# Kernel tuning notes

Hardware: AMD Instinct MI355X
Metric: run time of the kernel (lower is better)

Reference implementation:

```python
import jax, jax.numpy as jnp
import numpy as np
from jax import lax

START, STOP, NTAGS = 18, 19, 20
NEG = -10000.0
V, E, H, L = 100000, 300, 512, 512  # vocab, embed_dim, per-direction hidden, seq_len


def setup_inputs() -> dict:
    key = jax.random.key(0)
    ks = jax.random.split(key, 16)
    f = lambda k, s: jax.random.normal(k, s, dtype=jnp.float32) * 0.05
    trans = jax.random.normal(ks[14], (NTAGS, NTAGS), dtype=jnp.float32)
    trans = trans.at[START, :].set(NEG).at[:, STOP].set(NEG)
    return {
        "sentence": jax.random.randint(ks[0], (L,), 0, V),
        "embed_table": f(ks[1], (V, E)),
        "w_ih_f": f(ks[2], (4 * H, E)), "w_hh_f": f(ks[3], (4 * H, H)),
        "b_ih_f": f(ks[4], (4 * H,)), "b_hh_f": f(ks[5], (4 * H,)),
        "w_ih_b": f(ks[6], (4 * H, E)), "w_hh_b": f(ks[7], (4 * H, H)),
        "b_ih_b": f(ks[8], (4 * H,)), "b_hh_b": f(ks[9], (4 * H,)),
        "h0": f(ks[10], (2, H)), "c0": f(ks[11], (2, H)),
        "w_out": f(ks[12], (NTAGS, 2 * H)), "b_out": f(ks[13], (NTAGS,)),
        "transitions": trans,
    }


def _lstm_dir(x, wih, whh, bih, bhh, h0, c0, reverse):
    # x: [L, E]; PyTorch gate order i, f, g, o
    b = bih + bhh
    def step(carry, xt):
        h, c = carry
        g = xt @ wih.T + h @ whh.T + b  # [4H]
        i, fg, gg, o = jnp.split(g, 4)
        c = jax.nn.sigmoid(fg) * c + jax.nn.sigmoid(i) * jnp.tanh(gg)
        h = jax.nn.sigmoid(o) * jnp.tanh(c)
        return (h, c), h
    _, hs = lax.scan(step, (h0, c0), x, reverse=reverse)
    return hs  # [L, H] in time order


def _lstm_feats(sentence, embed_table, w_ih_f, w_hh_f, b_ih_f, b_hh_f,
                w_ih_b, w_hh_b, b_ih_b, b_hh_b, h0, c0, w_out, b_out):
    x = embed_table[sentence]  # [L, E]
    hf = _lstm_dir(x, w_ih_f, w_hh_f, b_ih_f, b_hh_f, h0[0], c0[0], False)
    hb = _lstm_dir(x, w_ih_b, w_hh_b, b_ih_b, b_hh_b, h0[1], c0[1], True)
    h = jnp.concatenate([hf, hb], axis=-1)  # [L, 2H]
    return h @ w_out.T + b_out  # [L, NTAGS]


def reference(sentence, embed_table, w_ih_f, w_hh_f, b_ih_f, b_hh_f,
              w_ih_b, w_hh_b, b_ih_b, b_hh_b, h0, c0, w_out, b_out, transitions):
    feats = _lstm_feats(sentence, embed_table, w_ih_f, w_hh_f, b_ih_f, b_hh_f,
                        w_ih_b, w_hh_b, b_ih_b, b_hh_b, h0, c0, w_out, b_out)
    init = jnp.full((NTAGS,), NEG, dtype=feats.dtype).at[START].set(0.0)

    def vstep(fv, feat):
        scores = fv[None, :] + transitions  # [next_tag, prev_tag]
        bptr = jnp.argmax(scores, axis=1)
        return jnp.max(scores, axis=1) + feat, bptr

    fv, bptrs = lax.scan(vstep, init, feats)  # bptrs: [L, NTAGS]
    terminal = fv + transitions[STOP]
    best = jnp.argmax(terminal)

    def back(tag, bp):
        # tag is the best tag at step t; bp maps tag_t -> tag_{t-1}
        return bp[tag], tag

    _, path = lax.scan(back, best, bptrs, reverse=True)  # [L] in time order
    return path
```

## Files before the change

kernel.cpp:

```cpp
#include <hip/hip_runtime.h>
#include <math.h>

typedef unsigned long long u64;
typedef unsigned int u32;

#define L 512
#define E 300
#define H 512
#define G4H 2048
#define NTAGS 20
#define START_TAG 18
#define STOP_TAG 19

#define KC 100

#define OFF_XW    0u
#define OFF_HIST  8388608u
#define OFF_HBUF  10485760u
#define OFF_FEATS 10502144u

__global__ __launch_bounds__(256) void k1_xw(
    const int* __restrict__ sentence, const float* __restrict__ embed,
    const float* __restrict__ wih_f, const float* __restrict__ wih_b,
    const float* __restrict__ bih_f, const float* __restrict__ bhh_f,
    const float* __restrict__ bih_b, const float* __restrict__ bhh_b,
    float* __restrict__ xw) {
    __shared__ float wST[KC][68];
    __shared__ float xST[KC][68];
    __shared__ int   sT[64];

    const int tid = threadIdx.x;
    const int tx = tid & 15;
    const int ty = tid >> 4;
    const int n_base = blockIdx.x * 64;
    const int t_base = blockIdx.y * 64;
    const int dir = blockIdx.z;
    const float* wih = dir ? wih_b : wih_f;
    const float* bih = dir ? bih_b : bih_f;
    const float* bhh = dir ? bhh_b : bhh_f;

    if (tid < 64) sT[tid] = sentence[t_base + tid];
    __syncthreads();

    float acc[4][4];
#pragma unroll
    for (int i = 0; i < 4; ++i)
#pragma unroll
        for (int j = 0; j < 4; ++j) acc[i][j] = 0.f;

    for (int kc = 0; kc < E; kc += KC) {
#pragma unroll
        for (int i = 0; i < 25; ++i) {
            int idx = i * 256 + tid;
            int row = idx / KC, col = idx % KC;
            wST[col][row] = wih[(size_t)(n_base + row) * E + kc + col];
        }
#pragma unroll
        for (int i = 0; i < 25; ++i) {
            int idx = i * 256 + tid;
            int trow = idx / KC, col = idx % KC;
            xST[col][trow] = embed[(size_t)sT[trow] * E + kc + col];
        }
        __syncthreads();

#pragma unroll 4
        for (int k = 0; k < KC; ++k) {
            float4 wv4 = *(const float4*)&wST[k][ty * 4];
            float4 xv4 = *(const float4*)&xST[k][tx * 4];
            float wv[4] = {wv4.x, wv4.y, wv4.z, wv4.w};
            float xv[4] = {xv4.x, xv4.y, xv4.z, xv4.w};
#pragma unroll
            for (int i = 0; i < 4; ++i)
#pragma unroll
                for (int j = 0; j < 4; ++j)
                    acc[i][j] = fmaf(wv[i], xv[j], acc[i][j]);
        }
        __syncthreads();
    }

#pragma unroll
    for (int i = 0; i < 4; ++i) {
        int n = n_base + ty * 4 + i;
        float b = bih[n] + bhh[n];
        int u = n & (H - 1), g = n >> 9;
        int pos = (u >> 4) * 64 + (u & 15) * 4 + g;
#pragma unroll
        for (int j = 0; j < 4; ++j) {
            int t = t_base + tx * 4 + j;
            xw[((size_t)(dir * L) + t) * G4H + pos] = acc[i][j] + b;
        }
    }
}

__global__ __launch_bounds__(512) void k2_lstm(
    const float* __restrict__ whh_f, const float* __restrict__ whh_b,
    const float* __restrict__ h0, const float* __restrict__ c0,
    const float* __restrict__ xw, float* __restrict__ hist,
    u64* __restrict__ hbuf) {
    const int bid = blockIdx.x;
    const int dir = bid >> 5;
    const int wg  = bid & 31;
    const int tid = threadIdx.x;
    const int wv  = tid >> 6;
    const int l   = tid & 63;
    const int jj  = l >> 2;
    const int g   = l & 3;
    const int grow = g * H + wg * 16 + jj;

    const float* whh = dir ? whh_b : whh_f;
    float* histd = hist + (size_t)dir * L * H;
    u64* hb = hbuf + dir * 1024;

    float w[64];
    {
        const float* wp = whh + (size_t)grow * H + wv * 64;
#pragma unroll
        for (int i = 0; i < 64; i += 4) {
            float4 v = *(const float4*)(wp + i);
            w[i] = v.x; w[i+1] = v.y; w[i+2] = v.z; w[i+3] = v.w;
        }
    }

    __shared__ float pbuf[2][8][68];

    float c = 0.f;
    if (l == 0 || l == 4) c = c0[dir * H + wg * 16 + 2 * wv + (l >> 2)];

    for (int s = 1; s <= L; ++s) {
        const int t = dir ? (L - s) : (s - 1);
        const int par = s & 1;

        float xwv = 0.f;
        if (l < 8)
            xwv = xw[((size_t)(dir * L) + t) * G4H + wg * 64 + wv * 8 + l];

        float hval;
        if (s == 1) {
            hval = h0[dir * H + tid];
        } else {
            u64* slot = hb + ((s - 1) & 1) * 512 + tid;
            u64 u;
            while (((u = __hip_atomic_load(slot, __ATOMIC_RELAXED,
                                           __HIP_MEMORY_SCOPE_AGENT)) >> 32)
                   != (u32)(s - 1)) { }
            hval = __uint_as_float((u32)u);
        }

        float a0 = 0.f, a1 = 0.f, a2 = 0.f, a3 = 0.f;
#pragma unroll
        for (int i = 0; i < 64; i += 4) {
            float h0v = __uint_as_float((u32)__builtin_amdgcn_readlane(
                            (int)__float_as_uint(hval), i));
            float h1v = __uint_as_float((u32)__builtin_amdgcn_readlane(
                            (int)__float_as_uint(hval), i + 1));
            float h2v = __uint_as_float((u32)__builtin_amdgcn_readlane(
                            (int)__float_as_uint(hval), i + 2));
            float h3v = __uint_as_float((u32)__builtin_amdgcn_readlane(
                            (int)__float_as_uint(hval), i + 3));
            a0 = fmaf(w[i],     h0v, a0);
            a1 = fmaf(w[i + 1], h1v, a1);
            a2 = fmaf(w[i + 2], h2v, a2);
            a3 = fmaf(w[i + 3], h3v, a3);
        }
        pbuf[par][wv][l] = (a0 + a1) + (a2 + a3);
        __syncthreads();

        float part = pbuf[par][l >> 3][8 * wv + (l & 7)];
        part += __shfl_xor(part, 8);
        part += __shfl_xor(part, 16);
        part += __shfl_xor(part, 32);
        float pre = part + xwv;
        float aa = (g == 2) ? 2.f * pre : pre;
        float sg = 1.f / (1.f + __expf(-aa));
        float vg = (g == 2) ? (2.f * sg - 1.f) : sg;
        float gi = __shfl(vg, (l & 4));
        float gf = __shfl(vg, (l & 4) + 1);
        float gg = __shfl(vg, (l & 4) + 2);
        float go = __shfl(vg, (l & 4) + 3);
        if (l == 0 || l == 4) {
            c = gf * c + gi * gg;
            float th = 2.f / (1.f + __expf(-2.f * c)) - 1.f;
            float hout = go * th;
            int u = wg * 16 + 2 * wv + (l >> 2);
            u64 e = ((u64)(u32)s << 32) | (u64)__float_as_uint(hout);
            __hip_atomic_store(hb + par * 512 + u, e,
                               __ATOMIC_RELAXED, __HIP_MEMORY_SCOPE_AGENT);
            histd[(size_t)t * H + u] = hout;
        }
    }
}

__global__ void k3_feats(const float* __restrict__ hist,
                         const float* __restrict__ wout,
                         const float* __restrict__ bout,
                         float* __restrict__ feats) {
    int t = blockIdx.x;
    int tid = threadIdx.x;
    int tag = tid >> 4;
    int part = tid & 15;
    const float* h0p = hist + (size_t)t * H;
    const float* h1p = hist + (size_t)L * H + (size_t)t * H;
    int j0 = part * 64;
    float acc = 0.f;
    for (int jj = 0; jj < 64; jj += 4) {
        int j = j0 + jj;
        float4 w4 = *(const float4*)(wout + (size_t)tag * (2 * H) + j);
        float4 h4 = (j < H) ? *(const float4*)(h0p + j)
                            : *(const float4*)(h1p + (j - H));
        acc = fmaf(w4.x, h4.x, fmaf(w4.y, h4.y,
              fmaf(w4.z, h4.z, fmaf(w4.w, h4.w, acc))));
    }
    acc += __shfl_xor(acc, 8, 16);
    acc += __shfl_xor(acc, 4, 16);
    acc += __shfl_xor(acc, 2, 16);
    acc += __shfl_xor(acc, 1, 16);
    if (part == 0) feats[(size_t)t * NTAGS + tag] = acc + bout[tag];
}

__global__ void k4_viterbi(const float* __restrict__ feats,
                           const float* __restrict__ trans,
                           int* __restrict__ out) {
    __shared__ unsigned char bp[L * NTAGS];
    int lane = threadIdx.x;
    bool act = lane < NTAGS;

    float trl[NTAGS];
#pragma unroll
    for (int p = 0; p < NTAGS; ++p)
        trl[p] = act ? trans[lane * NTAGS + p] : -1.0e30f;

    float fv = (lane == START_TAG) ? 0.f : -10000.f;
    float nf = act ? feats[lane] : 0.f;

    for (int t = 0; t < L; ++t) {
        float f = nf;
        if (act && t + 1 < L) nf = feats[(size_t)(t + 1) * NTAGS + lane];
        float tv[NTAGS];
        int   ti[NTAGS];
#pragma unroll
        for (int p = 0; p < NTAGS; ++p) {
            tv[p] = __shfl(fv, p) + trl[p];
            ti[p] = p;
        }
#pragma unroll
        for (int p = 0; p < 4; ++p) {
            bool take = (tv[p + 16] > tv[p]) ||
                        (tv[p + 16] == tv[p] && ti[p + 16] < ti[p]);
            if (take) { tv[p] = tv[p + 16]; ti[p] = ti[p + 16]; }
        }
#pragma unroll
        for (int w = 8; w >= 1; w >>= 1)
#pragma unroll
            for (int p = 0; p < 16; ++p) if (p < w) {
                bool take = (tv[p + w] > tv[p]) ||
                            (tv[p + w] == tv[p] && ti[p + w] < ti[p]);
                if (take) { tv[p] = tv[p + w]; ti[p] = ti[p + w]; }
            }
        fv = tv[0] + f;
        if (act) bp[t * NTAGS + lane] = (unsigned char)ti[0];
    }

    float ts = act ? fv + trans[STOP_TAG * NTAGS + lane] : -1.0e30f;
    int bi = lane;
#pragma unroll
    for (int off = 32; off; off >>= 1) {
        float ov = __shfl_down(ts, off);
        int   oi = __shfl_down(bi, off);
        if (ov > ts) { ts = ov; bi = oi; }
    }
    if (lane == 0) {
        int tag = bi;
        out[L - 1] = tag;
        for (int t = L - 1; t >= 1; --t) {
            tag = bp[t * NTAGS + tag];
            out[t - 1] = tag;
        }
    }
}

extern "C" void kernel_launch(void* const* d_in, const int* in_sizes, int n_in,
                              void* d_out, int out_size, void* d_ws, size_t ws_size,
                              hipStream_t stream) {
    const int*   sentence = (const int*)d_in[0];
    const float* embed    = (const float*)d_in[1];
    const float* wih_f    = (const float*)d_in[2];
    const float* whh_f    = (const float*)d_in[3];
    const float* bih_f    = (const float*)d_in[4];
    const float* bhh_f    = (const float*)d_in[5];
    const float* wih_b    = (const float*)d_in[6];
    const float* whh_b    = (const float*)d_in[7];
    const float* bih_b    = (const float*)d_in[8];
    const float* bhh_b    = (const float*)d_in[9];
    const float* h0       = (const float*)d_in[10];
    const float* c0       = (const float*)d_in[11];
    const float* wout     = (const float*)d_in[12];
    const float* bout     = (const float*)d_in[13];
    const float* trans    = (const float*)d_in[14];
    int* out = (int*)d_out;

    char* ws = (char*)d_ws;
    float* xw    = (float*)(ws + OFF_XW);
    float* hist  = (float*)(ws + OFF_HIST);
    float* feats = (float*)(ws + OFF_FEATS);
    u64*   hbuf  = (u64*)(ws + OFF_HBUF);

    k1_xw<<<dim3(32, 8, 2), 256, 0, stream>>>(sentence, embed, wih_f, wih_b,
                                              bih_f, bhh_f, bih_b, bhh_b, xw);
    k2_lstm<<<64, 512, 0, stream>>>(whh_f, whh_b, h0, c0, xw, hist, hbuf);
    k3_feats<<<L, 320, 0, stream>>>(hist, wout, bout, feats);
    k4_viterbi<<<1, 64, 0, stream>>>(feats, trans, out);
}
```

Measured before the change: 1.605 ms.

## Concentrate LSTM gate reduction in one wavefront and pipeline spin-wait loads

```diff
diff --git a/kernel.cpp b/kernel.cpp
--- a/kernel.cpp
+++ b/kernel.cpp
@@ -83,7 +83,7 @@
         int n = n_base + ty * 4 + i;
         float b = bih[n] + bhh[n];
         int u = n & (H - 1), g = n >> 9;
-        int pos = (u >> 4) * 64 + (u & 15) * 4 + g;
+        int pos = (u >> 4) * 64 + g * 16 + (u & 15);
 #pragma unroll
         for (int j = 0; j < 4; ++j) {
             int t = t_base + tx * 4 + j;
@@ -103,9 +103,9 @@
     const int tid = threadIdx.x;
     const int wv  = tid >> 6;
     const int l   = tid & 63;
-    const int jj  = l >> 2;
-    const int g   = l & 3;
-    const int grow = g * H + wg * 16 + jj;
+    const int g   = l >> 4;
+    const int j   = l & 15;
+    const int grow = g * H + wg * 16 + j;
 
     const float* whh = dir ? whh_b : whh_f;
     float* histd = hist + (size_t)dir * L * H;
@@ -123,27 +123,30 @@
 
     __shared__ float pbuf[2][8][68];
 
-    float c = 0.f;
-    if (l == 0 || l == 4) c = c0[dir * H + wg * 16 + 2 * wv + (l >> 2)];
+    float c = (tid < 16) ? c0[dir * H + wg * 16 + tid] : 0.f;
 
     for (int s = 1; s <= L; ++s) {
         const int t = dir ? (L - s) : (s - 1);
         const int par = s & 1;
 
         float xwv = 0.f;
-        if (l < 8)
-            xwv = xw[((size_t)(dir * L) + t) * G4H + wg * 64 + wv * 8 + l];
+        if (tid < 64)
+            xwv = xw[((size_t)(dir * L) + t) * G4H + wg * 64 + l];
 
         float hval;
         if (s == 1) {
             hval = h0[dir * H + tid];
         } else {
+            const u32 want = (u32)(s - 1);
             u64* slot = hb + ((s - 1) & 1) * 512 + tid;
-            u64 u;
-            while (((u = __hip_atomic_load(slot, __ATOMIC_RELAXED,
-                                           __HIP_MEMORY_SCOPE_AGENT)) >> 32)
-                   != (u32)(s - 1)) { }
-            hval = __uint_as_float((u32)u);
+            u64 v0 = __hip_atomic_load(slot, __ATOMIC_RELAXED, __HIP_MEMORY_SCOPE_AGENT);
+            u64 v1 = __hip_atomic_load(slot, __ATOMIC_RELAXED, __HIP_MEMORY_SCOPE_AGENT);
+            u64 v2 = __hip_atomic_load(slot, __ATOMIC_RELAXED, __HIP_MEMORY_SCOPE_AGENT);
+            while ((u32)(v0 >> 32) != want) {
+                v0 = v1; v1 = v2;
+                v2 = __hip_atomic_load(slot, __ATOMIC_RELAXED, __HIP_MEMORY_SCOPE_AGENT);
+            }
+            hval = __uint_as_float((u32)v0);
         }
 
         float a0 = 0.f, a1 = 0.f, a2 = 0.f, a3 = 0.f;
@@ -165,27 +168,27 @@
         pbuf[par][wv][l] = (a0 + a1) + (a2 + a3);
         __syncthreads();
 
-        float part = pbuf[par][l >> 3][8 * wv + (l & 7)];
-        part += __shfl_xor(part, 8);
-        part += __shfl_xor(part, 16);
-        part += __shfl_xor(part, 32);
-        float pre = part + xwv;
-        float aa = (g == 2) ? 2.f * pre : pre;
-        float sg = 1.f / (1.f + __expf(-aa));
-        float vg = (g == 2) ? (2.f * sg - 1.f) : sg;
-        float gi = __shfl(vg, (l & 4));
-        float gf = __shfl(vg, (l & 4) + 1);
-        float gg = __shfl(vg, (l & 4) + 2);
-        float go = __shfl(vg, (l & 4) + 3);
-        if (l == 0 || l == 4) {
-            c = gf * c + gi * gg;
-            float th = 2.f / (1.f + __expf(-2.f * c)) - 1.f;
-            float hout = go * th;
-            int u = wg * 16 + 2 * wv + (l >> 2);
-            u64 e = ((u64)(u32)s << 32) | (u64)__float_as_uint(hout);
-            __hip_atomic_store(hb + par * 512 + u, e,
-                               __ATOMIC_RELAXED, __HIP_MEMORY_SCOPE_AGENT);
-            histd[(size_t)t * H + u] = hout;
+        if (tid < 64) {
+            float tot = 0.f;
+#pragma unroll
+            for (int p = 0; p < 8; ++p) tot += pbuf[par][p][l];
+            float pre = tot + xwv;
+            float aa = (g == 2) ? 2.f * pre : pre;
+            float sg = 1.f / (1.f + __expf(-aa));
+            float vg = (g == 2) ? (2.f * sg - 1.f) : sg;
+            float gi = __shfl(vg, j);
+            float gf = __shfl(vg, 16 + j);
+            float gg = __shfl(vg, 32 + j);
+            float go = __shfl(vg, 48 + j);
+            if (tid < 16) {
+                c = gf * c + gi * gg;
+                float th = 2.f / (1.f + __expf(-2.f * c)) - 1.f;
+                float hout = go * th;
+                u64 e = ((u64)(u32)s << 32) | (u64)__float_as_uint(hout);
+                __hip_atomic_store(hb + par * 512 + wg * 16 + tid, e,
+                                   __ATOMIC_RELAXED, __HIP_MEMORY_SCOPE_AGENT);
+                histd[(size_t)t * H + wg * 16 + tid] = hout;
+            }
         }
     }
 }
```

Measured after the change: 1.365 ms. 14.9% less time.
